# Kernel optimization log

Measured on AMD Instinct MI355X. Metric: run time of the kernel, lower is better.

Reference implementation:

```python
import jax, jax.numpy as jnp
import numpy as np

N_NODES = 50000
N_EDGES = 800000
F_IN = 16
F_EDGE = 8
H = 8  # latent_dim = [8, 8]
NUM_GRAPHS = 512


def setup_inputs() -> dict:
    key = jax.random.key(0)
    ks = jax.random.split(key, 16)
    x = jax.random.normal(ks[0], (N_NODES, F_IN), dtype=jnp.float32)
    edge_index = jax.random.randint(ks[1], (2, N_EDGES), 0, N_NODES)
    edge_attr = jax.random.normal(ks[2], (N_EDGES, F_EDGE), dtype=jnp.float32)
    batch = jnp.sort(jax.random.randint(ks[3], (N_NODES,), 0, NUM_GRAPHS))
    s = 0.1
    # edge MLPs (single Linear each): edge_attr -> flattened [in, out] weight
    We1 = jax.random.normal(ks[4], (F_EDGE, F_IN * H), dtype=jnp.float32) * s
    be1 = jnp.zeros((F_IN * H,), dtype=jnp.float32)
    We2 = jax.random.normal(ks[5], (F_EDGE, H * H), dtype=jnp.float32) * s
    be2 = jnp.zeros((H * H,), dtype=jnp.float32)
    # NNConv root weights + biases
    root1 = jax.random.normal(ks[6], (F_IN, H), dtype=jnp.float32) * s
    b1 = jnp.zeros((H,), dtype=jnp.float32)
    root2 = jax.random.normal(ks[7], (H, H), dtype=jnp.float32) * s
    b2 = jnp.zeros((H,), dtype=jnp.float32)
    # final readout linear H -> 1
    Wlast = jax.random.normal(ks[8], (H, 1), dtype=jnp.float32) * s
    blast = jnp.zeros((1,), dtype=jnp.float32)
    return {"x": x, "edge_index": edge_index, "edge_attr": edge_attr, "batch": batch,
            "We1": We1, "be1": be1, "root1": root1, "b1": b1,
            "We2": We2, "be2": be2, "root2": root2, "b2": b2,
            "Wlast": Wlast, "blast": blast}


def _nnconv(x, src, dst, edge_attr, We, be, root, b, in_dim, out_dim):
    # per-edge weight matrix from edge MLP: [E, in_dim, out_dim]
    W = (edge_attr @ We + be).reshape(-1, in_dim, out_dim)
    # gather source features, per-edge matvec, scatter-add to targets
    msg = jnp.einsum('ei,eio->eo', x[src], W)            # [E, out_dim]
    agg = jax.ops.segment_sum(msg, dst, num_segments=x.shape[0])
    return agg + x @ root + b                            # root weight + bias


def reference(x, edge_index, edge_attr, batch, We1, be1, root1, b1,
              We2, be2, root2, b2, Wlast, blast):
    src, dst = edge_index[0], edge_index[1]
    h = jax.nn.relu(_nnconv(x, src, dst, edge_attr, We1, be1, root1, b1, F_IN, H))
    h = jax.nn.relu(_nnconv(h, src, dst, edge_attr, We2, be2, root2, b2, H, H))
    # per-graph sum pooling (vectorized equivalent of the python loop)
    pooled = jax.ops.segment_sum(h, batch, num_segments=NUM_GRAPHS)  # [G, H]
    return pooled @ Wlast + blast                                    # [G, 1]
```

## Files before the change

kernel.cpp:

```cpp
#include <hip/hip_runtime.h>

#define F_EDGE 8
#define H 8

__device__ __forceinline__ unsigned short f2bf(float f) {
    unsigned u = __float_as_uint(f);
    unsigned r = u + 0x7fffu + ((u >> 16) & 1u);
    return (unsigned short)(r >> 16);
}
__device__ __forceinline__ float bflo(unsigned u) { return __uint_as_float(u << 16); }
__device__ __forceinline__ float bfhi(unsigned u) { return __uint_as_float(u & 0xffff0000u); }

__global__ void init_out_kernel(float* __restrict__ out,
                                const float* __restrict__ blast, int n) {
    int g = blockIdx.x * blockDim.x + threadIdx.x;
    if (g < n) out[g] = blast[0];
}

template <int IN, bool RELU>
__global__ __launch_bounds__(256) void prep_kernel(
    const float* __restrict__ feat,
    const float* __restrict__ We,
    const float* __restrict__ be,
    const float* __restrict__ root,
    const float* __restrict__ b,
    unsigned short* __restrict__ Pt,
    float* __restrict__ q,
    float* __restrict__ aggseed,
    int n_nodes) {
    __shared__ float sW[IN * H * 12];
    int tid = threadIdx.x;
    for (int t = tid; t < IN * H * 12; t += 256) {
        int r = t / 12, m = t - r * 12;
        float v = 0.f;
        if (m < 8) v = We[m * (IN * H) + r];
        else if (m == 8) v = be[r];
        else if (m == 9) v = root[r];
        sW[t] = v;
    }
    __syncthreads();

    int n = blockIdx.x * 32 + (tid >> 3);
    if (n >= n_nodes) return;
    int j = tid & 7;

    float f[IN];
    const float4* fv = (const float4*)(feat + (long long)n * IN);
#pragma unroll
    for (int i4 = 0; i4 < IN / 4; ++i4) {
        float4 v = fv[i4];
        f[i4 * 4 + 0] = v.x; f[i4 * 4 + 1] = v.y;
        f[i4 * 4 + 2] = v.z; f[i4 * 4 + 3] = v.w;
    }
    if (RELU) {
#pragma unroll
        for (int i = 0; i < IN; ++i) f[i] = f[i] > 0.f ? f[i] : 0.f;
    }

    float p[8] = {0.f, 0.f, 0.f, 0.f, 0.f, 0.f, 0.f, 0.f};
    float qq = 0.f, hr = 0.f;
#pragma unroll
    for (int i = 0; i < IN; ++i) {
        const float* row = &sW[(i * 8 + j) * 12];
        float4 w0 = *(const float4*)row;
        float4 w1 = *(const float4*)(row + 4);
        float2 br = *(const float2*)(row + 8);
        float fi = f[i];
        p[0] = fmaf(fi, w0.x, p[0]); p[1] = fmaf(fi, w0.y, p[1]);
        p[2] = fmaf(fi, w0.z, p[2]); p[3] = fmaf(fi, w0.w, p[3]);
        p[4] = fmaf(fi, w1.x, p[4]); p[5] = fmaf(fi, w1.y, p[5]);
        p[6] = fmaf(fi, w1.z, p[6]); p[7] = fmaf(fi, w1.w, p[7]);
        qq = fmaf(fi, br.x, qq);
        hr = fmaf(fi, br.y, hr);
    }
    uint4 pw;
    pw.x = (unsigned)f2bf(p[0]) | ((unsigned)f2bf(p[1]) << 16);
    pw.y = (unsigned)f2bf(p[2]) | ((unsigned)f2bf(p[3]) << 16);
    pw.z = (unsigned)f2bf(p[4]) | ((unsigned)f2bf(p[5]) << 16);
    pw.w = (unsigned)f2bf(p[6]) | ((unsigned)f2bf(p[7]) << 16);
    *(uint4*)(Pt + ((long long)n * H + j) * F_EDGE) = pw;
    q[(long long)n * H + j] = qq;
    aggseed[(long long)n * H + j] = hr + b[j];
}

__global__ __launch_bounds__(256) void edge_fact_kernel(
    const int* __restrict__ ei,
    const float* __restrict__ ea,
    const unsigned short* __restrict__ Pt,
    const float* __restrict__ q,
    float* __restrict__ agg,
    int E) {
    long long gid = (long long)blockIdx.x * blockDim.x + threadIdx.x;
    int e = (int)(gid >> 3);
    if (e >= E) return;
    int j = (int)(gid & 7);

    int src = ei[e];
    int dst = ei[E + e];

    const float4* av = (const float4*)(ea + (long long)e * F_EDGE);
    float4 a0 = av[0], a1 = av[1];

    uint4 pw = *(const uint4*)(Pt + ((long long)src * H + j) * F_EDGE);

    float m = q[(long long)src * H + j];
    m = fmaf(a0.x, bflo(pw.x), m);
    m = fmaf(a0.y, bfhi(pw.x), m);
    m = fmaf(a0.z, bflo(pw.y), m);
    m = fmaf(a0.w, bfhi(pw.y), m);
    m = fmaf(a1.x, bflo(pw.z), m);
    m = fmaf(a1.y, bfhi(pw.z), m);
    m = fmaf(a1.z, bflo(pw.w), m);
    m = fmaf(a1.w, bfhi(pw.w), m);

    unsafeAtomicAdd(&agg[(long long)dst * H + j], m);
}

__global__ __launch_bounds__(256) void pool_kernel(
    const float* __restrict__ h2pre, const int* __restrict__ batch,
    const float* __restrict__ Wlast, float* __restrict__ out,
    int n_nodes, int n_graphs) {
    __shared__ float bins[512];
    bool use_bins = (n_graphs <= 512);
    if (use_bins) {
        for (int t = threadIdx.x; t < n_graphs; t += 256) bins[t] = 0.f;
        __syncthreads();
    }
    float wl[8];
#pragma unroll
    for (int j = 0; j < 8; ++j) wl[j] = Wlast[j];

    int base = blockIdx.x * 1024;
#pragma unroll
    for (int r = 0; r < 4; ++r) {
        int n = base + r * 256 + threadIdx.x;
        if (n < n_nodes) {
            const float4* hv = (const float4*)(h2pre + (long long)n * H);
            float4 h0 = hv[0], h1 = hv[1];
            float c = 0.f;
            c = fmaf(fmaxf(h0.x, 0.f), wl[0], c);
            c = fmaf(fmaxf(h0.y, 0.f), wl[1], c);
            c = fmaf(fmaxf(h0.z, 0.f), wl[2], c);
            c = fmaf(fmaxf(h0.w, 0.f), wl[3], c);
            c = fmaf(fmaxf(h1.x, 0.f), wl[4], c);
            c = fmaf(fmaxf(h1.y, 0.f), wl[5], c);
            c = fmaf(fmaxf(h1.z, 0.f), wl[6], c);
            c = fmaf(fmaxf(h1.w, 0.f), wl[7], c);
            if (use_bins) atomicAdd(&bins[batch[n]], c);
            else unsafeAtomicAdd(&out[batch[n]], c);
        }
    }
    if (use_bins) {
        __syncthreads();
        for (int t = threadIdx.x; t < n_graphs; t += 256) {
            float v = bins[t];
            if (v != 0.f) unsafeAtomicAdd(&out[t], v);
        }
    }
}

extern "C" void kernel_launch(void* const* d_in, const int* in_sizes, int n_in,
                              void* d_out, int out_size, void* d_ws, size_t ws_size,
                              hipStream_t stream) {
    const float* x     = (const float*)d_in[0];
    const int*   ei    = (const int*)d_in[1];
    const float* ea    = (const float*)d_in[2];
    const int*   batch = (const int*)d_in[3];
    const float* We1   = (const float*)d_in[4];
    const float* be1   = (const float*)d_in[5];
    const float* root1 = (const float*)d_in[6];
    const float* b1    = (const float*)d_in[7];
    const float* We2   = (const float*)d_in[8];
    const float* be2   = (const float*)d_in[9];
    const float* root2 = (const float*)d_in[10];
    const float* b2    = (const float*)d_in[11];
    const float* Wlast = (const float*)d_in[12];
    const float* blast = (const float*)d_in[13];
    float* out = (float*)d_out;

    int F_IN_rt = 16;
    int n_nodes = in_sizes[0] / F_IN_rt;
    int E = in_sizes[1] / 2;

    size_t nH = (size_t)n_nodes * H;
    unsigned short* Pt1 = (unsigned short*)d_ws;
    unsigned short* Pt2 = Pt1 + (size_t)n_nodes * H * F_EDGE;
    float* q1    = (float*)(Pt2 + (size_t)n_nodes * H * F_EDGE);
    float* q2    = q1 + nH;
    float* h1pre = q2 + nH;
    float* h2pre = h1pre + nH;

    init_out_kernel<<<(out_size + 255) / 256, 256, 0, stream>>>(out, blast, out_size);

    int nblocks = (n_nodes + 31) / 32;
    prep_kernel<16, false><<<nblocks, 256, 0, stream>>>(
        x, We1, be1, root1, b1, Pt1, q1, h1pre, n_nodes);

    long long lanes = (long long)E * H;
    int eblks = (int)((lanes + 255) / 256);
    edge_fact_kernel<<<eblks, 256, 0, stream>>>(ei, ea, Pt1, q1, h1pre, E);

    prep_kernel<H, true><<<nblocks, 256, 0, stream>>>(
        h1pre, We2, be2, root2, b2, Pt2, q2, h2pre, n_nodes);

    edge_fact_kernel<<<eblks, 256, 0, stream>>>(ei, ea, Pt2, q2, h2pre, E);

    int pblocks = (n_nodes + 1023) / 1024;
    pool_kernel<<<pblocks, 256, 0, stream>>>(h2pre, batch, Wlast, out, n_nodes, out_size);
}
```

Measured before the change: 197.6 us.

## Build dst-sorted CSR per call and replace atomic scatter with pull aggregation

Each call builds a destination-sorted CSR using a histogram, a three-pass scan and an atomic scatter that also permutes the edge attributes. The two per-layer edge kernels that scattered with float atomics become a per-node pull kernel, one wave per node with shuffle reduction. This removes float atomic contention in the edge layers. In exchange it adds several kernels, integer atomics and a full extra pass over the edge data on every call.

```diff
diff --git a/kernel.cpp b/kernel.cpp
--- a/kernel.cpp
+++ b/kernel.cpp
@@ -17,17 +17,88 @@
     if (g < n) out[g] = blast[0];
 }
 
+__global__ void zero_int_kernel(int* __restrict__ p, int n) {
+    int i = blockIdx.x * blockDim.x + threadIdx.x;
+    if (i < n) p[i] = 0;
+}
+
+__global__ __launch_bounds__(256) void hist_kernel(const int* __restrict__ ei,
+                                                   int* __restrict__ cnt, int E) {
+    int e = blockIdx.x * blockDim.x + threadIdx.x;
+    if (e < E) atomicAdd(&cnt[ei[E + e]], 1);
+}
+
+__global__ __launch_bounds__(256) void scan1_kernel(const int* __restrict__ cnt,
+                                                    int* __restrict__ excl,
+                                                    int* __restrict__ bsum, int n) {
+    __shared__ int s[256];
+    int tid = threadIdx.x;
+    int gid = blockIdx.x * 256 + tid;
+    int v = (gid < n) ? cnt[gid] : 0;
+    s[tid] = v;
+    __syncthreads();
+#pragma unroll
+    for (int off = 1; off < 256; off <<= 1) {
+        int t = (tid >= off) ? s[tid - off] : 0;
+        __syncthreads();
+        s[tid] += t;
+        __syncthreads();
+    }
+    if (gid < n) excl[gid] = s[tid] - v;
+    if (tid == 255) bsum[blockIdx.x] = s[255];
+}
+
+__global__ __launch_bounds__(256) void scan2_kernel(const int* __restrict__ bsum,
+                                                    int* __restrict__ bsumx, int nb) {
+    __shared__ int s[256];
+    int tid = threadIdx.x;
+    int v = (tid < nb) ? bsum[tid] : 0;
+    s[tid] = v;
+    __syncthreads();
+#pragma unroll
+    for (int off = 1; off < 256; off <<= 1) {
+        int t = (tid >= off) ? s[tid - off] : 0;
+        __syncthreads();
+        s[tid] += t;
+        __syncthreads();
+    }
+    if (tid < nb) bsumx[tid] = s[tid] - v;
+}
+
+__global__ __launch_bounds__(256) void scan3_kernel(const int* __restrict__ excl,
+                                                    const int* __restrict__ bsumx,
+                                                    int* __restrict__ row_start,
+                                                    int* __restrict__ cursor, int n) {
+    int i = blockIdx.x * 256 + threadIdx.x;
+    if (i < n) {
+        int v = excl[i] + bsumx[blockIdx.x];
+        row_start[i] = v;
+        cursor[i] = v;
+    }
+}
+
+__global__ __launch_bounds__(256) void scatter_kernel(
+    const int* __restrict__ ei, const float* __restrict__ ea,
+    int* __restrict__ cursor, int* __restrict__ src_s,
+    float* __restrict__ ea_s, int E) {
+    int e = blockIdx.x * blockDim.x + threadIdx.x;
+    if (e >= E) return;
+    int src = ei[e];
+    int dst = ei[E + e];
+    int pos = atomicAdd(&cursor[dst], 1);
+    src_s[pos] = src;
+    const float4* av = (const float4*)(ea + (size_t)e * F_EDGE);
+    float4* ov = (float4*)(ea_s + (size_t)pos * F_EDGE);
+    ov[0] = av[0];
+    ov[1] = av[1];
+}
+
 template <int IN, bool RELU>
 __global__ __launch_bounds__(256) void prep_kernel(
-    const float* __restrict__ feat,
-    const float* __restrict__ We,
-    const float* __restrict__ be,
-    const float* __restrict__ root,
-    const float* __restrict__ b,
-    unsigned short* __restrict__ Pt,
-    float* __restrict__ q,
-    float* __restrict__ aggseed,
-    int n_nodes) {
+    const float* __restrict__ feat, const float* __restrict__ We,
+    const float* __restrict__ be, const float* __restrict__ root,
+    const float* __restrict__ b, unsigned short* __restrict__ Pt,
+    float* __restrict__ q, float* __restrict__ seed, int n_nodes) {
     __shared__ float sW[IN * H * 12];
     int tid = threadIdx.x;
     for (int t = tid; t < IN * H * 12; t += 256) {
@@ -80,40 +151,50 @@
     pw.w = (unsigned)f2bf(p[6]) | ((unsigned)f2bf(p[7]) << 16);
     *(uint4*)(Pt + ((long long)n * H + j) * F_EDGE) = pw;
     q[(long long)n * H + j] = qq;
-    aggseed[(long long)n * H + j] = hr + b[j];
-}
-
-__global__ __launch_bounds__(256) void edge_fact_kernel(
-    const int* __restrict__ ei,
-    const float* __restrict__ ea,
-    const unsigned short* __restrict__ Pt,
-    const float* __restrict__ q,
-    float* __restrict__ agg,
-    int E) {
-    long long gid = (long long)blockIdx.x * blockDim.x + threadIdx.x;
-    int e = (int)(gid >> 3);
-    if (e >= E) return;
-    int j = (int)(gid & 7);
-
-    int src = ei[e];
-    int dst = ei[E + e];
-
-    const float4* av = (const float4*)(ea + (long long)e * F_EDGE);
-    float4 a0 = av[0], a1 = av[1];
-
-    uint4 pw = *(const uint4*)(Pt + ((long long)src * H + j) * F_EDGE);
-
-    float m = q[(long long)src * H + j];
-    m = fmaf(a0.x, bflo(pw.x), m);
-    m = fmaf(a0.y, bfhi(pw.x), m);
-    m = fmaf(a0.z, bflo(pw.y), m);
-    m = fmaf(a0.w, bfhi(pw.y), m);
-    m = fmaf(a1.x, bflo(pw.z), m);
-    m = fmaf(a1.y, bfhi(pw.z), m);
-    m = fmaf(a1.z, bflo(pw.w), m);
-    m = fmaf(a1.w, bfhi(pw.w), m);
-
-    unsafeAtomicAdd(&agg[(long long)dst * H + j], m);
+    seed[(long long)n * H + j] = hr + b[j];
+}
+
+__global__ __launch_bounds__(256) void agg_csr_kernel(
+    const int* __restrict__ row_start, const int* __restrict__ cnt,
+    const int* __restrict__ src_s, const float* __restrict__ ea_s,
+    const unsigned short* __restrict__ Pt, const float* __restrict__ q,
+    float* __restrict__ feat_io,
+    int n_nodes) {
+    int wave = threadIdx.x >> 6;
+    int lane = threadIdx.x & 63;
+    int n = blockIdx.x * 4 + wave;
+    if (n >= n_nodes) return;
+    int ee = lane >> 3, j = lane & 7;
+
+    int start = row_start[n];
+    int end = start + cnt[n];
+    float acc = 0.f;
+    for (int base = start; base < end; base += 8) {
+        int idx = base + ee;
+        if (idx < end) {
+            int src = src_s[idx];
+            const float4* av = (const float4*)(ea_s + (size_t)idx * F_EDGE);
+            float4 a0 = av[0], a1 = av[1];
+            uint4 pw = *(const uint4*)(Pt + ((size_t)src * H + j) * F_EDGE);
+            float m = q[(size_t)src * H + j];
+            m = fmaf(a0.x, bflo(pw.x), m);
+            m = fmaf(a0.y, bfhi(pw.x), m);
+            m = fmaf(a0.z, bflo(pw.y), m);
+            m = fmaf(a0.w, bfhi(pw.y), m);
+            m = fmaf(a1.x, bflo(pw.z), m);
+            m = fmaf(a1.y, bfhi(pw.z), m);
+            m = fmaf(a1.z, bflo(pw.w), m);
+            m = fmaf(a1.w, bfhi(pw.w), m);
+            acc += m;
+        }
+    }
+    acc += __shfl_xor(acc, 8, 64);
+    acc += __shfl_xor(acc, 16, 64);
+    acc += __shfl_xor(acc, 32, 64);
+    if (ee == 0) {
+        size_t o = (size_t)n * H + j;
+        feat_io[o] = feat_io[o] + acc;
+    }
 }
 
 __global__ __launch_bounds__(256) void pool_kernel(
@@ -178,33 +259,53 @@
     const float* blast = (const float*)d_in[13];
     float* out = (float*)d_out;
 
-    int F_IN_rt = 16;
-    int n_nodes = in_sizes[0] / F_IN_rt;
+    int n_nodes = in_sizes[0] / 16;
     int E = in_sizes[1] / 2;
-
-    size_t nH = (size_t)n_nodes * H;
-    unsigned short* Pt1 = (unsigned short*)d_ws;
-    unsigned short* Pt2 = Pt1 + (size_t)n_nodes * H * F_EDGE;
-    float* q1    = (float*)(Pt2 + (size_t)n_nodes * H * F_EDGE);
-    float* q2    = q1 + nH;
-    float* h1pre = q2 + nH;
-    float* h2pre = h1pre + nH;
+    int nb = (n_nodes + 255) / 256;
+
+    char* w = (char*)d_ws;
+    auto carve = [&](size_t bytes) {
+        char* p = w;
+        w += (bytes + 15) & ~(size_t)15;
+        return p;
+    };
+    unsigned short* Pt1 = (unsigned short*)carve((size_t)n_nodes * 64 * 2);
+    unsigned short* Pt2 = (unsigned short*)carve((size_t)n_nodes * 64 * 2);
+    float* q1    = (float*)carve((size_t)n_nodes * 8 * 4);
+    float* q2    = (float*)carve((size_t)n_nodes * 8 * 4);
+    float* h1pre = (float*)carve((size_t)n_nodes * 8 * 4);
+    float* h2pre = (float*)carve((size_t)n_nodes * 8 * 4);
+    int* cnt       = (int*)carve((size_t)n_nodes * 4);
+    int* excl      = (int*)carve((size_t)n_nodes * 4);
+    int* row_start = (int*)carve((size_t)n_nodes * 4);
+    int* cursor    = (int*)carve((size_t)n_nodes * 4);
+    int* bsum      = (int*)carve((size_t)nb * 4);
+    int* bsumx     = (int*)carve((size_t)nb * 4);
+    int* src_s     = (int*)carve((size_t)E * 4);
+    float* ea_s    = (float*)carve((size_t)E * F_EDGE * 4);
 
     init_out_kernel<<<(out_size + 255) / 256, 256, 0, stream>>>(out, blast, out_size);
 
-    int nblocks = (n_nodes + 31) / 32;
-    prep_kernel<16, false><<<nblocks, 256, 0, stream>>>(
+    zero_int_kernel<<<nb, 256, 0, stream>>>(cnt, n_nodes);
+    hist_kernel<<<(E + 255) / 256, 256, 0, stream>>>(ei, cnt, E);
+    scan1_kernel<<<nb, 256, 0, stream>>>(cnt, excl, bsum, n_nodes);
+    scan2_kernel<<<1, 256, 0, stream>>>(bsum, bsumx, nb);
+    scan3_kernel<<<nb, 256, 0, stream>>>(excl, bsumx, row_start, cursor, n_nodes);
+    scatter_kernel<<<(E + 255) / 256, 256, 0, stream>>>(ei, ea, cursor, src_s, ea_s, E);
+
+    int pblocks = (n_nodes + 31) / 32;
+    int ablocks = (n_nodes + 3) / 4;
+
+    prep_kernel<16, false><<<pblocks, 256, 0, stream>>>(
         x, We1, be1, root1, b1, Pt1, q1, h1pre, n_nodes);
-
-    long long lanes = (long long)E * H;
-    int eblks = (int)((lanes + 255) / 256);
-    edge_fact_kernel<<<eblks, 256, 0, stream>>>(ei, ea, Pt1, q1, h1pre, E);
-
-    prep_kernel<H, true><<<nblocks, 256, 0, stream>>>(
+    agg_csr_kernel<<<ablocks, 256, 0, stream>>>(
+        row_start, cnt, src_s, ea_s, Pt1, q1, h1pre, n_nodes);
+
+    prep_kernel<8, true><<<pblocks, 256, 0, stream>>>(
         h1pre, We2, be2, root2, b2, Pt2, q2, h2pre, n_nodes);
-
-    edge_fact_kernel<<<eblks, 256, 0, stream>>>(ei, ea, Pt2, q2, h2pre, E);
-
-    int pblocks = (n_nodes + 1023) / 1024;
-    pool_kernel<<<pblocks, 256, 0, stream>>>(h2pre, batch, Wlast, out, n_nodes, out_size);
-}
+    agg_csr_kernel<<<ablocks, 256, 0, stream>>>(
+        row_start, cnt, src_s, ea_s, Pt2, q2, h2pre, n_nodes);
+
+    pool_kernel<<<(n_nodes + 1023) / 1024, 256, 0, stream>>>(
+        h2pre, batch, Wlast, out, n_nodes, out_size);
+}
```

Result: slower. 263.2 us (+33.2%).

## Pack edge records in bf16 and aggregate with packed fp16 atomics

Applied to the files above, without the earlier changes.

Adds a pre-pass that interleaves src, dst and bf16-packed edge attributes into a 24-byte record per edge, which both edge passes then read. Each edge thread now computes two output channels and issues a single packed half2 atomic add. Node aggregates are stored in fp16 rather than fp32, which halves atomic traffic and node-feature reads. In exchange it adds an extra kernel and loses precision from fp16 accumulation across many atomic adds and from bf16 edge attributes.

```diff
diff --git a/kernel.cpp b/kernel.cpp
--- a/kernel.cpp
+++ b/kernel.cpp
@@ -1,4 +1,5 @@
 #include <hip/hip_runtime.h>
+#include <hip/hip_fp16.h>
 
 #define F_EDGE 8
 #define H 8
@@ -17,17 +18,33 @@
     if (g < n) out[g] = blast[0];
 }
 
-template <int IN, bool RELU>
+__global__ __launch_bounds__(256) void pack_edges_kernel(
+    const int* __restrict__ ei, const float* __restrict__ ea,
+    uint2* __restrict__ rec, int E) {
+    int e = blockIdx.x * blockDim.x + threadIdx.x;
+    if (e >= E) return;
+    uint2 hdr;
+    hdr.x = (unsigned)ei[e];
+    hdr.y = (unsigned)ei[E + e];
+    const float4* av = (const float4*)(ea + (size_t)e * F_EDGE);
+    float4 a0 = av[0], a1 = av[1];
+    uint2 p0, p1;
+    p0.x = (unsigned)f2bf(a0.x) | ((unsigned)f2bf(a0.y) << 16);
+    p0.y = (unsigned)f2bf(a0.z) | ((unsigned)f2bf(a0.w) << 16);
+    p1.x = (unsigned)f2bf(a1.x) | ((unsigned)f2bf(a1.y) << 16);
+    p1.y = (unsigned)f2bf(a1.z) | ((unsigned)f2bf(a1.w) << 16);
+    size_t b = (size_t)e * 3;
+    rec[b] = hdr;
+    rec[b + 1] = p0;
+    rec[b + 2] = p1;
+}
+
+template <int IN, bool RELU, bool F16IN>
 __global__ __launch_bounds__(256) void prep_kernel(
-    const float* __restrict__ feat,
-    const float* __restrict__ We,
-    const float* __restrict__ be,
-    const float* __restrict__ root,
-    const float* __restrict__ b,
-    unsigned short* __restrict__ Pt,
-    float* __restrict__ q,
-    float* __restrict__ aggseed,
-    int n_nodes) {
+    const void* __restrict__ featv, const float* __restrict__ We,
+    const float* __restrict__ be, const float* __restrict__ root,
+    const float* __restrict__ b, unsigned short* __restrict__ Pt,
+    float* __restrict__ q, __half* __restrict__ seedh, int n_nodes) {
     __shared__ float sW[IN * H * 12];
     int tid = threadIdx.x;
     for (int t = tid; t < IN * H * 12; t += 256) {
@@ -45,12 +62,25 @@
     int j = tid & 7;
 
     float f[IN];
-    const float4* fv = (const float4*)(feat + (long long)n * IN);
-#pragma unroll
-    for (int i4 = 0; i4 < IN / 4; ++i4) {
-        float4 v = fv[i4];
-        f[i4 * 4 + 0] = v.x; f[i4 * 4 + 1] = v.y;
-        f[i4 * 4 + 2] = v.z; f[i4 * 4 + 3] = v.w;
+    if (F16IN) {
+        const uint4* fv = (const uint4*)((const unsigned short*)featv + (size_t)n * IN);
+        uint4 v = fv[0];
+        unsigned w[4] = {v.x, v.y, v.z, v.w};
+#pragma unroll
+        for (int p = 0; p < 4 && 2 * p + 1 < IN; ++p) {
+            __half2 h2v = *(__half2*)&w[p];
+            float2 ff = __half22float2(h2v);
+            f[2 * p] = ff.x;
+            f[2 * p + 1] = ff.y;
+        }
+    } else {
+        const float4* fv = (const float4*)((const float*)featv + (size_t)n * IN);
+#pragma unroll
+        for (int i4 = 0; i4 < IN / 4; ++i4) {
+            float4 v = fv[i4];
+            f[i4 * 4 + 0] = v.x; f[i4 * 4 + 1] = v.y;
+            f[i4 * 4 + 2] = v.z; f[i4 * 4 + 3] = v.w;
+        }
     }
     if (RELU) {
 #pragma unroll
@@ -80,44 +110,54 @@
     pw.w = (unsigned)f2bf(p[6]) | ((unsigned)f2bf(p[7]) << 16);
     *(uint4*)(Pt + ((long long)n * H + j) * F_EDGE) = pw;
     q[(long long)n * H + j] = qq;
-    aggseed[(long long)n * H + j] = hr + b[j];
+    seedh[(long long)n * H + j] = __float2half(hr + b[j]);
 }
 
 __global__ __launch_bounds__(256) void edge_fact_kernel(
-    const int* __restrict__ ei,
-    const float* __restrict__ ea,
+    const uint2* __restrict__ rec,
     const unsigned short* __restrict__ Pt,
     const float* __restrict__ q,
-    float* __restrict__ agg,
+    __half* __restrict__ agg,
     int E) {
     long long gid = (long long)blockIdx.x * blockDim.x + threadIdx.x;
-    int e = (int)(gid >> 3);
+    int e = (int)(gid >> 2);
     if (e >= E) return;
-    int j = (int)(gid & 7);
-
-    int src = ei[e];
-    int dst = ei[E + e];
-
-    const float4* av = (const float4*)(ea + (long long)e * F_EDGE);
-    float4 a0 = av[0], a1 = av[1];
-
-    uint4 pw = *(const uint4*)(Pt + ((long long)src * H + j) * F_EDGE);
-
-    float m = q[(long long)src * H + j];
-    m = fmaf(a0.x, bflo(pw.x), m);
-    m = fmaf(a0.y, bfhi(pw.x), m);
-    m = fmaf(a0.z, bflo(pw.y), m);
-    m = fmaf(a0.w, bfhi(pw.y), m);
-    m = fmaf(a1.x, bflo(pw.z), m);
-    m = fmaf(a1.y, bfhi(pw.z), m);
-    m = fmaf(a1.z, bflo(pw.w), m);
-    m = fmaf(a1.w, bfhi(pw.w), m);
-
-    unsafeAtomicAdd(&agg[(long long)dst * H + j], m);
+    int jj = (int)(gid & 3);
+
+    size_t rb = (size_t)e * 3;
+    uint2 hdr = rec[rb];
+    uint2 A = rec[rb + 1];
+    uint2 B = rec[rb + 2];
+    int src = (int)hdr.x;
+    int dst = (int)hdr.y;
+
+    float a0 = bflo(A.x), a1 = bfhi(A.x), a2 = bflo(A.y), a3 = bfhi(A.y);
+    float a4 = bflo(B.x), a5 = bfhi(B.x), a6 = bflo(B.y), a7 = bfhi(B.y);
+
+    const uint4* pp = (const uint4*)(Pt + (size_t)src * 64 + jj * 16);
+    uint4 lo = pp[0];
+    uint4 hi = pp[1];
+
+    float2 q2 = *(const float2*)(q + (size_t)src * H + jj * 2);
+
+    float m0 = q2.x;
+    m0 = fmaf(a0, bflo(lo.x), m0); m0 = fmaf(a1, bfhi(lo.x), m0);
+    m0 = fmaf(a2, bflo(lo.y), m0); m0 = fmaf(a3, bfhi(lo.y), m0);
+    m0 = fmaf(a4, bflo(lo.z), m0); m0 = fmaf(a5, bfhi(lo.z), m0);
+    m0 = fmaf(a6, bflo(lo.w), m0); m0 = fmaf(a7, bfhi(lo.w), m0);
+
+    float m1 = q2.y;
+    m1 = fmaf(a0, bflo(hi.x), m1); m1 = fmaf(a1, bfhi(hi.x), m1);
+    m1 = fmaf(a2, bflo(hi.y), m1); m1 = fmaf(a3, bfhi(hi.y), m1);
+    m1 = fmaf(a4, bflo(hi.z), m1); m1 = fmaf(a5, bfhi(hi.z), m1);
+    m1 = fmaf(a6, bflo(hi.w), m1); m1 = fmaf(a7, bfhi(hi.w), m1);
+
+    __half2* ap = (__half2*)agg + ((size_t)dst * 4 + jj);
+    unsafeAtomicAdd(ap, __floats2half2_rn(m0, m1));
 }
 
 __global__ __launch_bounds__(256) void pool_kernel(
-    const float* __restrict__ h2pre, const int* __restrict__ batch,
+    const unsigned short* __restrict__ h2, const int* __restrict__ batch,
     const float* __restrict__ Wlast, float* __restrict__ out,
     int n_nodes, int n_graphs) {
     __shared__ float bins[512];
@@ -135,17 +175,15 @@
     for (int r = 0; r < 4; ++r) {
         int n = base + r * 256 + threadIdx.x;
         if (n < n_nodes) {
-            const float4* hv = (const float4*)(h2pre + (long long)n * H);
-            float4 h0 = hv[0], h1 = hv[1];
+            uint4 v = *(const uint4*)(h2 + (size_t)n * H);
+            unsigned w[4] = {v.x, v.y, v.z, v.w};
             float c = 0.f;
-            c = fmaf(fmaxf(h0.x, 0.f), wl[0], c);
-            c = fmaf(fmaxf(h0.y, 0.f), wl[1], c);
-            c = fmaf(fmaxf(h0.z, 0.f), wl[2], c);
-            c = fmaf(fmaxf(h0.w, 0.f), wl[3], c);
-            c = fmaf(fmaxf(h1.x, 0.f), wl[4], c);
-            c = fmaf(fmaxf(h1.y, 0.f), wl[5], c);
-            c = fmaf(fmaxf(h1.z, 0.f), wl[6], c);
-            c = fmaf(fmaxf(h1.w, 0.f), wl[7], c);
+#pragma unroll
+            for (int p = 0; p < 4; ++p) {
+                float2 ff = __half22float2(*(__half2*)&w[p]);
+                c = fmaf(fmaxf(ff.x, 0.f), wl[2 * p], c);
+                c = fmaf(fmaxf(ff.y, 0.f), wl[2 * p + 1], c);
+            }
             if (use_bins) atomicAdd(&bins[batch[n]], c);
             else unsafeAtomicAdd(&out[batch[n]], c);
         }
@@ -178,33 +216,40 @@
     const float* blast = (const float*)d_in[13];
     float* out = (float*)d_out;
 
-    int F_IN_rt = 16;
-    int n_nodes = in_sizes[0] / F_IN_rt;
+    int n_nodes = in_sizes[0] / 16;
     int E = in_sizes[1] / 2;
 
-    size_t nH = (size_t)n_nodes * H;
-    unsigned short* Pt1 = (unsigned short*)d_ws;
-    unsigned short* Pt2 = Pt1 + (size_t)n_nodes * H * F_EDGE;
-    float* q1    = (float*)(Pt2 + (size_t)n_nodes * H * F_EDGE);
-    float* q2    = q1 + nH;
-    float* h1pre = q2 + nH;
-    float* h2pre = h1pre + nH;
+    char* w = (char*)d_ws;
+    auto carve = [&](size_t bytes) {
+        char* p = w;
+        w += (bytes + 15) & ~(size_t)15;
+        return p;
+    };
+    unsigned short* Pt1 = (unsigned short*)carve((size_t)n_nodes * 64 * 2);
+    unsigned short* Pt2 = (unsigned short*)carve((size_t)n_nodes * 64 * 2);
+    float* q1 = (float*)carve((size_t)n_nodes * 8 * 4);
+    float* q2 = (float*)carve((size_t)n_nodes * 8 * 4);
+    __half* h1 = (__half*)carve((size_t)n_nodes * 8 * 2);
+    __half* h2 = (__half*)carve((size_t)n_nodes * 8 * 2);
+    uint2* rec = (uint2*)carve((size_t)E * 24);
 
     init_out_kernel<<<(out_size + 255) / 256, 256, 0, stream>>>(out, blast, out_size);
 
+    pack_edges_kernel<<<(E + 255) / 256, 256, 0, stream>>>(ei, ea, rec, E);
+
     int nblocks = (n_nodes + 31) / 32;
-    prep_kernel<16, false><<<nblocks, 256, 0, stream>>>(
-        x, We1, be1, root1, b1, Pt1, q1, h1pre, n_nodes);
-
-    long long lanes = (long long)E * H;
+    prep_kernel<16, false, false><<<nblocks, 256, 0, stream>>>(
+        x, We1, be1, root1, b1, Pt1, q1, h1, n_nodes);
+
+    long long lanes = (long long)E * 4;
     int eblks = (int)((lanes + 255) / 256);
-    edge_fact_kernel<<<eblks, 256, 0, stream>>>(ei, ea, Pt1, q1, h1pre, E);
-
-    prep_kernel<H, true><<<nblocks, 256, 0, stream>>>(
-        h1pre, We2, be2, root2, b2, Pt2, q2, h2pre, n_nodes);
-
-    edge_fact_kernel<<<eblks, 256, 0, stream>>>(ei, ea, Pt2, q2, h2pre, E);
-
-    int pblocks = (n_nodes + 1023) / 1024;
-    pool_kernel<<<pblocks, 256, 0, stream>>>(h2pre, batch, Wlast, out, n_nodes, out_size);
-}
+    edge_fact_kernel<<<eblks, 256, 0, stream>>>(rec, Pt1, q1, h1, E);
+
+    prep_kernel<8, true, true><<<nblocks, 256, 0, stream>>>(
+        h1, We2, be2, root2, b2, Pt2, q2, h2, n_nodes);
+
+    edge_fact_kernel<<<eblks, 256, 0, stream>>>(rec, Pt2, q2, h2, E);
+
+    pool_kernel<<<(n_nodes + 1023) / 1024, 256, 0, stream>>>(
+        (const unsigned short*)h2, batch, Wlast, out, n_nodes, out_size);
+}
```

After: 206.1 us. 1.04x slower.
